# Kernel optimization log

Measured on AMD Instinct MI355X. Metric: run time of the kernel, lower is better.

## Reference

```python
import jax, jax.numpy as jnp
import numpy as np

B, C, D = 8192, 1000, 128
ALPHA = 0.5      # margin scale
LAMBDA = 0.5     # likelihood-margin weight
LAM2 = 0.1       # SCL weight
T = 0.3          # SCL temperature


def l2_normalized(x):
    # matches F.normalize(p=2, dim=1) with eps clamp
    n = jnp.maximum(jnp.linalg.norm(x, axis=1, keepdims=True), 1e-12)
    return x / n


def scl_loss(feat, labels, t):
    # vectorized form of the original O(B^2) python double loop
    sim = jnp.matmul(feat, feat.T) / t                     # [B, B]
    eye = jnp.eye(feat.shape[0], dtype=bool)
    exp_sim = jnp.where(eye, 0.0, jnp.exp(sim))
    bottom = exp_sim.sum(axis=1)                            # [B] denominator over k != i
    log_ratio = sim - jnp.log(bottom)[:, None]              # log(exp(sim_ij)/bottom_i)
    pos = (labels[:, None] == labels[None, :]) & (~eye)     # same-label pairs, j != i
    cnt = pos.sum(axis=1)
    sum_log = jnp.where(pos, log_ratio, 0.0).sum(axis=1)
    valid = cnt > 0
    per_i = jnp.where(valid, sum_log / jnp.maximum(cnt, 1), 0.0)
    n_sample = valid.sum()
    return -per_i.sum() / jnp.maximum(n_sample, 1)


def setup_inputs() -> dict:
    key = jax.random.key(0)
    k1, k2, k3 = jax.random.split(key, 3)
    feat = jax.random.normal(k1, (B, D), dtype=jnp.float32)
    labels = jax.random.randint(k2, (B,), 0, C, dtype=jnp.int64)
    # xavier_uniform_ with gain sqrt(2): bound = gain * sqrt(6/(fan_in+fan_out))
    bound = np.sqrt(2.0) * np.sqrt(6.0 / (C + D))
    means = jax.random.uniform(k3, (C, D), dtype=jnp.float32, minval=-bound, maxval=bound)
    return {"feat": feat, "labels": labels, "means": means}


def reference(feat, labels, means):
    feat_n = l2_normalized(feat)                            # scl=True path
    # neg squared distance to (unnormalized) means
    XY = jnp.matmul(feat_n, means.T)                        # [B, C]
    XX = (feat_n ** 2).sum(axis=1, keepdims=True)           # [B, 1]
    YY = (means ** 2).sum(axis=1)[None, :]                  # [1, C]
    neg_sqr_dist = -0.5 * (XX - 2.0 * XY + YY)

    # margin logits: multiply true-class logit by (1 + alpha)
    K = 1.0 + ALPHA * jax.nn.one_hot(labels, C, dtype=neg_sqr_dist.dtype)
    logits = neg_sqr_dist * K
    log_p = jax.nn.log_softmax(logits, axis=1)
    ce = -log_p[jnp.arange(B), labels].mean()

    means_n = l2_normalized(means)                          # scl=True normalizes means too
    means_batch = means_n[labels]                           # [B, D]
    loss_margin = ((feat_n - means_batch) ** 2).sum() / 2.0 / B

    scl = scl_loss(feat_n, labels, T)
    loss = (1.0 - LAM2) * ce + LAM2 * scl + LAMBDA * loss_margin
    return neg_sqr_dist, loss
```

## Files before the change

### kernel.cpp

```cpp
#include <hip/hip_runtime.h>
#include <math.h>

#define BN 8192
#define CN 1000
#define DN 128
#define INVT (1.0f/0.3f)
#define EXP2C 4.80898346962988f

typedef __bf16 bf16x8 __attribute__((ext_vector_type(8)));
typedef float  f32x4  __attribute__((ext_vector_type(4)));

#define F_FEATN  0
#define F_MEANSN 1048576
#define F_XX     1176576
#define F_YY     1184768
#define F_DIAG   1185768
#define F_FEATB  1193960
#define F_MEANSB 1718248
#define F_PL     1808360
#define F_BOT    1939432
#define F_CNT    1947624
#define F_CSUM   1948624
#define F_RED    2076624
#define NZERO    (8192 + 1000 + 128000 + 4)

#define NB_FEAT  2048
#define NB_MEANS 256
#define NB_ZERO  64

#define NB_SCL  576
#define NB_NSD  1024
#define NB_CSUM 512

__device__ __forceinline__ void async16(const void* g, void* s) {
    __builtin_amdgcn_global_load_lds(
        (const __attribute__((address_space(1))) void*)g,
        (__attribute__((address_space(3))) void*)s, 16, 0, 0);
}

__global__ void norm_all(const float* __restrict__ feat, const float* __restrict__ means,
                         float* __restrict__ featn, float* __restrict__ meansn,
                         float* __restrict__ xx, float* __restrict__ yy,
                         __bf16* __restrict__ featb, __bf16* __restrict__ meansb,
                         float* __restrict__ diag, const int* __restrict__ labels,
                         int* __restrict__ counts, float* __restrict__ zbase) {
    int bx = blockIdx.x;
    int lane = threadIdx.x & 63;
    if (bx < NB_FEAT) {
        int row = bx * 4 + (threadIdx.x >> 6);
        float f0 = feat[row * DN + lane];
        float f1 = feat[row * DN + 64 + lane];
        float ss = f0 * f0 + f1 * f1;
        #pragma unroll
        for (int o = 32; o > 0; o >>= 1) ss += __shfl_xor(ss, o);
        float inv = 1.0f / fmaxf(sqrtf(ss), 1e-12f);
        float n0 = f0 * inv, n1 = f1 * inv;
        featn[row * DN + lane] = n0;
        featn[row * DN + 64 + lane] = n1;
        __bf16 b0 = (__bf16)n0, b1 = (__bf16)n1;
        featb[row * DN + lane] = b0;
        featb[row * DN + 64 + lane] = b1;
        float fb0 = (float)b0, fb1 = (float)b1;
        float sb = fb0 * fb0 + fb1 * fb1;
        #pragma unroll
        for (int o = 32; o > 0; o >>= 1) sb += __shfl_xor(sb, o);
        if (lane == 0) {
            diag[row] = sb;
            xx[row] = ss * inv * inv;
            atomicAdd(&counts[labels[row]], 1);
        }
    } else if (bx < NB_FEAT + NB_MEANS) {
        int row = (bx - NB_FEAT) * 4 + (threadIdx.x >> 6);
        float f0 = (row < CN) ? means[row * DN + lane] : 0.f;
        float f1 = (row < CN) ? means[row * DN + 64 + lane] : 0.f;
        meansb[row * DN + lane] = (__bf16)f0;
        meansb[row * DN + 64 + lane] = (__bf16)f1;
        if (row >= CN) return;
        float ss = f0 * f0 + f1 * f1;
        #pragma unroll
        for (int o = 32; o > 0; o >>= 1) ss += __shfl_xor(ss, o);
        float inv = 1.0f / fmaxf(sqrtf(ss), 1e-12f);
        meansn[row * DN + lane] = f0 * inv;
        meansn[row * DN + 64 + lane] = f1 * inv;
        if (lane == 0) yy[row] = ss;
    } else {
        int b2 = bx - NB_FEAT - NB_MEANS;
        for (int idx = b2 * 256 + (int)threadIdx.x; idx < NZERO; idx += NB_ZERO * 256) {
            float* p = zbase + idx;
            if (idx < 8192 || idx >= 9192) *p = 0.f;
        }
    }
}

__global__ __launch_bounds__(256, 3) void mega_kernel(
        const __bf16* __restrict__ featb, const __bf16* __restrict__ meansb,
        const float* __restrict__ featn, const int* __restrict__ labels,
        const float* __restrict__ xx, const float* __restrict__ yy,
        float* __restrict__ out, float* __restrict__ pl,
        float* __restrict__ bottom, float* __restrict__ csum) {
    __shared__ uint4 sh[2048];
    int bx = blockIdx.x;
    int tid = threadIdx.x;
    int lane = tid & 63, w = tid >> 6;
    int q = lane >> 4, l15 = lane & 15;
    int wrow = (w >> 1) * 32, wcol = (w & 1) * 64;

    auto stageA = [&](const uint4* src, int row0) {
        #pragma unroll
        for (int s = 0; s < 8; s++) {
            int rb = w * 32 + s * 4;
            int r = rb + q;
            async16(&src[(size_t)(row0 + r) * 16 + (l15 ^ (r & 7))], &sh[rb * 16]);
        }
    };

    if (bx < NB_SCL) {
        int rem = bx, a = 0;
        while (true) { int ns = (64 - (a >> 1) + 7) >> 3; if (rem < ns) break; rem -= ns; ++a; }
        int A = a >> 1;
        int J0 = A + rem * 8;
        int len = min(8, 64 - J0);
        int i0 = a * 64;
        const uint4* fv = (const uint4*)featb;

        bf16x8 af[2][4];
        #pragma unroll
        for (int ii = 0; ii < 2; ii++) {
            size_t r = (size_t)(i0 + wrow + ii * 16 + l15) * 16;
            #pragma unroll
            for (int kk = 0; kk < 4; kk++)
                af[ii][kk] = *(const bf16x8*)&fv[r + kk * 4 + q];
        }
        float bs[2][4] = {};

        for (int t = 0; t < len; t++) {
            int J = J0 + t;
            int j0 = J * 128;
            __syncthreads();
            stageA(fv, j0);
            __syncthreads();

            f32x4 acc[2][4];
            #pragma unroll
            for (int ii = 0; ii < 2; ii++)
                #pragma unroll
                for (int jj = 0; jj < 4; jj++) acc[ii][jj] = (f32x4){0.f, 0.f, 0.f, 0.f};
            #pragma unroll
            for (int kk = 0; kk < 4; kk++) {
                bf16x8 bfv[4];
                #pragma unroll
                for (int jj = 0; jj < 4; jj++) {
                    int r = wcol + jj * 16 + l15;
                    bfv[jj] = *(const bf16x8*)&sh[r * 16 + ((kk * 4 + q) ^ (r & 7))];
                }
                #pragma unroll
                for (int ii = 0; ii < 2; ii++)
                    #pragma unroll
                    for (int jj = 0; jj < 4; jj++)
                        acc[ii][jj] = __builtin_amdgcn_mfma_f32_16x16x32_bf16(
                            af[ii][kk], bfv[jj], acc[ii][jj], 0, 0, 0);
            }

            float cp[4] = {0.f, 0.f, 0.f, 0.f};
            #pragma unroll
            for (int ii = 0; ii < 2; ii++)
                #pragma unroll
                for (int jj = 0; jj < 4; jj++)
                    #pragma unroll
                    for (int r4 = 0; r4 < 4; r4++) {
                        float e = exp2f(acc[ii][jj][r4] * EXP2C);
                        bs[ii][r4] += e;
                        cp[jj] += e;
                    }
            if (J != A) {
                #pragma unroll
                for (int jj = 0; jj < 4; jj++) {
                    float c = cp[jj];
                    c += __shfl_xor(c, 16);
                    c += __shfl_xor(c, 32);
                    if (lane < 16)
                        atomicAdd(&bottom[j0 + wcol + jj * 16 + l15], c);
                }
            }
        }
        int ibase = i0 + wrow + q * 4;
        #pragma unroll
        for (int ii = 0; ii < 2; ii++)
            #pragma unroll
            for (int r4 = 0; r4 < 4; r4++) {
                float b = bs[ii][r4];
                #pragma unroll
                for (int o = 8; o > 0; o >>= 1) b += __shfl_xor(b, o);
                if (l15 == 0) atomicAdd(&bottom[ibase + ii * 16 + r4], b);
            }

    } else if (bx < NB_SCL + NB_NSD) {
        int b = bx - NB_SCL;
        int i0 = (b >> 3) * 64, j0 = (b & 7) * 128;
        const uint4* fv = (const uint4*)featb;
        stageA((const uint4*)meansb, j0);

        bf16x8 af[2][4];
        #pragma unroll
        for (int ii = 0; ii < 2; ii++) {
            size_t r = (size_t)(i0 + wrow + ii * 16 + l15) * 16;
            #pragma unroll
            for (int kk = 0; kk < 4; kk++)
                af[ii][kk] = *(const bf16x8*)&fv[r + kk * 4 + q];
        }
        __syncthreads();

        f32x4 acc[2][4];
        #pragma unroll
        for (int ii = 0; ii < 2; ii++)
            #pragma unroll
            for (int jj = 0; jj < 4; jj++) acc[ii][jj] = (f32x4){0.f, 0.f, 0.f, 0.f};
        #pragma unroll
        for (int kk = 0; kk < 4; kk++) {
            bf16x8 bfv[4];
            #pragma unroll
            for (int jj = 0; jj < 4; jj++) {
                int r = wcol + jj * 16 + l15;
                bfv[jj] = *(const bf16x8*)&sh[r * 16 + ((kk * 4 + q) ^ (r & 7))];
            }
            #pragma unroll
            for (int ii = 0; ii < 2; ii++)
                #pragma unroll
                for (int jj = 0; jj < 4; jj++)
                    acc[ii][jj] = __builtin_amdgcn_mfma_f32_16x16x32_bf16(
                        af[ii][kk], bfv[jj], acc[ii][jj], 0, 0, 0);
        }
        int jg[4]; float yv[4];
        #pragma unroll
        for (int jj = 0; jj < 4; jj++) {
            jg[jj] = j0 + wcol + jj * 16 + l15;
            yv[jj] = (jg[jj] < CN) ? yy[jg[jj]] : 0.f;
        }
        int pslot = ((b & 7) * 2 + (w & 1)) * BN;
        int ibase = i0 + wrow + q * 4;
        #pragma unroll
        for (int ii = 0; ii < 2; ii++) {
            int rbase = ibase + ii * 16;
            float4 xv = ((const float4*)xx)[rbase >> 2];
            int4 lv = ((const int4*)labels)[rbase >> 2];
            float xa[4] = {xv.x, xv.y, xv.z, xv.w};
            int la[4] = {lv.x, lv.y, lv.z, lv.w};
            #pragma unroll
            for (int r4 = 0; r4 < 4; r4++) {
                int ig = rbase + r4;
                float s = 0.f;
                #pragma unroll
                for (int jj = 0; jj < 4; jj++) {
                    float v = -0.5f * (xa[r4] - 2.f * acc[ii][jj][r4] + yv[jj]);
                    bool ok = (jg[jj] < CN);
                    if (ok) out[(size_t)ig * CN + jg[jj]] = v;
                    float l = (jg[jj] == la[r4]) ? 1.5f * v : v;
                    s += ok ? __expf(l) : 0.f;
                }
                #pragma unroll
                for (int o = 8; o > 0; o >>= 1) s += __shfl_xor(s, o);
                if (l15 == 0) pl[pslot + ig] = s;
            }
        }

    } else {
        int b2 = bx - NB_SCL - NB_NSD;
        for (int idx = b2 * 256 + tid; idx < BN * DN; idx += NB_CSUM * 256) {
            int row = idx >> 7, d = idx & 127;
            atomicAdd(&csum[labels[row] * DN + d], featn[idx]);
        }
    }
}

__global__ void cemp_kernel(const float* __restrict__ featn, const float* __restrict__ meansn,
        const float* __restrict__ csum, const int* __restrict__ labels,
        const float* __restrict__ pl, const float* __restrict__ out,
        const float* __restrict__ bottom, const int* __restrict__ counts,
        const float* __restrict__ diag, const float* __restrict__ xx,
        float* __restrict__ red) {
    int tid = threadIdx.x;
    int lane = tid & 63, w = tid >> 6;
    float a_sp = 0.f, a_nv = 0.f, a_ce = 0.f, a_mg = 0.f;
    for (int pass = 0; pass < 4; pass++) {
        int row = blockIdx.x * 16 + pass * 4 + w;
        int lab = labels[row];
        float f0 = featn[row * DN + lane],  f1 = featn[row * DN + 64 + lane];
        float m0 = meansn[lab * DN + lane], m1 = meansn[lab * DN + 64 + lane];
        float c0 = csum[lab * DN + lane],   c1 = csum[lab * DN + 64 + lane];
        float d0 = f0 - m0, d1 = f1 - m1;
        float ss = d0 * d0 + d1 * d1;
        float pp = f0 * c0 + f1 * c1;
        #pragma unroll
        for (int o = 32; o > 0; o >>= 1) {
            ss += __shfl_xor(ss, o);
            pp += __shfl_xor(pp, o);
        }
        if (lane == 0) {
            float S = 0.f;
            #pragma unroll
            for (int k = 0; k < 16; k++) S += pl[k * BN + row];
            a_ce += __logf(S) - 1.5f * out[(size_t)row * CN + lab];
            a_mg += ss;
            float bot = bottom[row] - __expf(diag[row] * INVT);
            float pv = (pp - xx[row]) * INVT;
            int c = counts[lab] - 1;
            if (c > 0) {
                a_sp += pv / (float)c - __logf(bot);
                a_nv += 1.f;
            }
        }
    }
    __shared__ float r4[4][4];
    if (lane == 0) { r4[w][0] = a_sp; r4[w][1] = a_nv; r4[w][2] = a_ce; r4[w][3] = a_mg; }
    __syncthreads();
    if (tid < 4)
        atomicAdd(&red[tid], r4[0][tid] + r4[1][tid] + r4[2][tid] + r4[3][tid]);
}

__global__ void final_fin(const float* __restrict__ red, float* __restrict__ loss_out) {
    float SP = red[0], NV = red[1], CE = red[2], MG = red[3];
    float scl = -SP / fmaxf(NV, 1.f);
    loss_out[0] = 0.9f * (CE / (float)BN) + 0.1f * scl + 0.5f * (MG / (2.f * (float)BN));
}

extern "C" void kernel_launch(void* const* d_in, const int* in_sizes, int n_in,
                              void* d_out, int out_size, void* d_ws, size_t ws_size,
                              hipStream_t stream) {
    const float* feat   = (const float*)d_in[0];
    const int*   labels = (const int*)d_in[1];
    const float* means  = (const float*)d_in[2];
    float* out = (float*)d_out;
    float* ws  = (float*)d_ws;

    float*  featn  = ws + F_FEATN;
    float*  meansn = ws + F_MEANSN;
    float*  xx     = ws + F_XX;
    float*  yy     = ws + F_YY;
    float*  diag   = ws + F_DIAG;
    __bf16* featb  = (__bf16*)(ws + F_FEATB);
    __bf16* meansb = (__bf16*)(ws + F_MEANSB);
    float*  pl     = ws + F_PL;
    float*  bottom = ws + F_BOT;
    int*    counts = (int*)(ws + F_CNT);
    float*  csum   = ws + F_CSUM;
    float*  red    = ws + F_RED;

    hipMemsetAsync(counts, 0, 1000 * sizeof(int), stream);

    norm_all<<<NB_FEAT + NB_MEANS + NB_ZERO, 256, 0, stream>>>(
        feat, means, featn, meansn, xx, yy, featb, meansb, diag, labels, counts,
        ws + F_BOT);
    mega_kernel<<<NB_SCL + NB_NSD + NB_CSUM, 256, 0, stream>>>(
        featb, meansb, featn, labels, xx, yy, out, pl, bottom, csum);
    cemp_kernel<<<512, 256, 0, stream>>>(featn, meansn, csum, labels, pl, out,
                                         bottom, counts, diag, xx, red);
    final_fin<<<1, 1, 0, stream>>>(red, out + (size_t)BN * CN);
}
```

Baseline: 123.2 us.

## Double-buffer SCL tile loads in 64-row halves with async prefetch

The SCL Gram loop now splits each 128-column tile into two 64-row halves held in two LDS buffers. The next half is prefetched with async loads while MFMA and exp work runs on the current one, replacing the two full __syncthreads per tile with partial vmcnt waits and raw barriers. This aims to hide global-to-LDS latency behind compute. In exchange each half-tile issues fewer MFMAs per barrier and needs more atomics per column. The NSD path is adapted to the split buffer layout.

After: 124.8 us. No clear change (+1.3%).

```diff
diff --git a/kernel.cpp b/kernel.cpp
--- a/kernel.cpp
+++ b/kernel.cpp
@@ -86,8 +86,7 @@
     } else {
         int b2 = bx - NB_FEAT - NB_MEANS;
         for (int idx = b2 * 256 + (int)threadIdx.x; idx < NZERO; idx += NB_ZERO * 256) {
-            float* p = zbase + idx;
-            if (idx < 8192 || idx >= 9192) *p = 0.f;
+            if (idx < 8192 || idx >= 9192) zbase[idx] = 0.f;
         }
     }
 }
@@ -98,19 +97,19 @@
         const float* __restrict__ xx, const float* __restrict__ yy,
         float* __restrict__ out, float* __restrict__ pl,
         float* __restrict__ bottom, float* __restrict__ csum) {
-    __shared__ uint4 sh[2048];
+    __shared__ uint4 sh[2][1024];
     int bx = blockIdx.x;
     int tid = threadIdx.x;
     int lane = tid & 63, w = tid >> 6;
     int q = lane >> 4, l15 = lane & 15;
-    int wrow = (w >> 1) * 32, wcol = (w & 1) * 64;
-
-    auto stageA = [&](const uint4* src, int row0) {
-        #pragma unroll
-        for (int s = 0; s < 8; s++) {
-            int rb = w * 32 + s * 4;
+    int wrow = (w >> 1) * 32;
+
+    auto stage64 = [&](const uint4* src, int row0, int buf) {
+        #pragma unroll
+        for (int s = 0; s < 4; s++) {
+            int rb = w * 16 + s * 4;
             int r = rb + q;
-            async16(&src[(size_t)(row0 + r) * 16 + (l15 ^ (r & 7))], &sh[rb * 16]);
+            async16(&src[(size_t)(row0 + r) * 16 + (l15 ^ (r & 7))], &sh[buf][rb * 16]);
         }
     };
 
@@ -122,6 +121,7 @@
         int len = min(8, 64 - J0);
         int i0 = a * 64;
         const uint4* fv = (const uint4*)featb;
+        int wc = (w & 1) * 32;
 
         bf16x8 af[2][4];
         #pragma unroll
@@ -133,55 +133,60 @@
         }
         float bs[2][4] = {};
 
-        for (int t = 0; t < len; t++) {
-            int J = J0 + t;
-            int j0 = J * 128;
-            __syncthreads();
-            stageA(fv, j0);
-            __syncthreads();
-
-            f32x4 acc[2][4];
+        int nh = 2 * len;
+        stage64(fv, J0 * 128, 0);
+        stage64(fv, J0 * 128 + 64, 1);
+
+        for (int h = 0; h < nh; h++) {
+            if (h + 1 < nh) asm volatile("s_waitcnt vmcnt(4)" ::: "memory");
+            else            asm volatile("s_waitcnt vmcnt(0)" ::: "memory");
+            __builtin_amdgcn_s_barrier();
+            const uint4* B = sh[h & 1];
+
+            f32x4 acc[2][2];
             #pragma unroll
             for (int ii = 0; ii < 2; ii++)
                 #pragma unroll
-                for (int jj = 0; jj < 4; jj++) acc[ii][jj] = (f32x4){0.f, 0.f, 0.f, 0.f};
+                for (int jj = 0; jj < 2; jj++) acc[ii][jj] = (f32x4){0.f, 0.f, 0.f, 0.f};
             #pragma unroll
             for (int kk = 0; kk < 4; kk++) {
-                bf16x8 bfv[4];
-                #pragma unroll
-                for (int jj = 0; jj < 4; jj++) {
-                    int r = wcol + jj * 16 + l15;
-                    bfv[jj] = *(const bf16x8*)&sh[r * 16 + ((kk * 4 + q) ^ (r & 7))];
+                bf16x8 bfv[2];
+                #pragma unroll
+                for (int jj = 0; jj < 2; jj++) {
+                    int r = wc + jj * 16 + l15;
+                    bfv[jj] = *(const bf16x8*)&B[r * 16 + ((kk * 4 + q) ^ (r & 7))];
                 }
                 #pragma unroll
                 for (int ii = 0; ii < 2; ii++)
                     #pragma unroll
-                    for (int jj = 0; jj < 4; jj++)
+                    for (int jj = 0; jj < 2; jj++)
                         acc[ii][jj] = __builtin_amdgcn_mfma_f32_16x16x32_bf16(
                             af[ii][kk], bfv[jj], acc[ii][jj], 0, 0, 0);
             }
 
-            float cp[4] = {0.f, 0.f, 0.f, 0.f};
+            float cp[2] = {0.f, 0.f};
             #pragma unroll
             for (int ii = 0; ii < 2; ii++)
                 #pragma unroll
-                for (int jj = 0; jj < 4; jj++)
+                for (int jj = 0; jj < 2; jj++)
                     #pragma unroll
                     for (int r4 = 0; r4 < 4; r4++) {
                         float e = exp2f(acc[ii][jj][r4] * EXP2C);
                         bs[ii][r4] += e;
                         cp[jj] += e;
                     }
-            if (J != A) {
-                #pragma unroll
-                for (int jj = 0; jj < 4; jj++) {
+            if (J0 + (h >> 1) != A) {
+                #pragma unroll
+                for (int jj = 0; jj < 2; jj++) {
                     float c = cp[jj];
                     c += __shfl_xor(c, 16);
                     c += __shfl_xor(c, 32);
                     if (lane < 16)
-                        atomicAdd(&bottom[j0 + wcol + jj * 16 + l15], c);
+                        atomicAdd(&bottom[J0 * 128 + h * 64 + wc + jj * 16 + l15], c);
                 }
             }
+            __builtin_amdgcn_s_barrier();
+            if (h + 2 < nh) stage64(fv, J0 * 128 + (h + 2) * 64, h & 1);
         }
         int ibase = i0 + wrow + q * 4;
         #pragma unroll
@@ -198,8 +203,11 @@
         int b = bx - NB_SCL;
         int i0 = (b >> 3) * 64, j0 = (b & 7) * 128;
         const uint4* fv = (const uint4*)featb;
-        stageA((const uint4*)meansb, j0);
-
+        const uint4* mv = (const uint4*)meansb;
+        stage64(mv, j0, 0);
+        stage64(mv, j0 + 64, 1);
+
+        int wcol = (w & 1) * 64;
         bf16x8 af[2][4];
         #pragma unroll
         for (int ii = 0; ii < 2; ii++) {
@@ -209,6 +217,7 @@
                 af[ii][kk] = *(const bf16x8*)&fv[r + kk * 4 + q];
         }
         __syncthreads();
+        const uint4* B = sh[w & 1];
 
         f32x4 acc[2][4];
         #pragma unroll
@@ -220,8 +229,8 @@
             bf16x8 bfv[4];
             #pragma unroll
             for (int jj = 0; jj < 4; jj++) {
-                int r = wcol + jj * 16 + l15;
-                bfv[jj] = *(const bf16x8*)&sh[r * 16 + ((kk * 4 + q) ^ (r & 7))];
+                int rl = jj * 16 + l15;
+                bfv[jj] = *(const bf16x8*)&B[rl * 16 + ((kk * 4 + q) ^ (rl & 7))];
             }
             #pragma unroll
             for (int ii = 0; ii < 2; ii++)
```
